# Kernel optimization log

Measured on AMD Instinct MI355X. Metric: run time of the kernel, lower is better.

Reference implementation:

```python
import jax, jax.numpy as jnp
import numpy as np

D = 1024
B, N = 4, 2048

def setup_inputs() -> dict:
    key = jax.random.key(0)
    ks = jax.random.split(key, 7)
    sc = 1.0 / np.sqrt(D)
    return {
        "x": jax.random.normal(ks[0], (B, N, D), dtype=jnp.float32),
        "wq_w": jax.random.normal(ks[1], (D, D), dtype=jnp.float32) * sc,
        "wq_b": jax.random.normal(ks[2], (D,), dtype=jnp.float32) * 0.01,
        "wk_w": jax.random.normal(ks[3], (D, D), dtype=jnp.float32) * sc,
        "wk_b": jax.random.normal(ks[4], (D,), dtype=jnp.float32) * 0.01,
        "wv_w": jax.random.normal(ks[5], (D, D), dtype=jnp.float32) * sc,
        "wv_b": jax.random.normal(ks[6], (D,), dtype=jnp.float32) * 0.01,
    }

def reference(x, wq_w, wq_b, wk_w, wk_b, wv_w, wv_b):
    # torch Linear: y = x @ W^T + b
    q = x @ wq_w.T + wq_b
    k = x @ wk_w.T + wk_b
    v = x @ wv_w.T + wv_b
    d = q.shape[-1]
    s = jnp.einsum("bid,bjd->bij", q, k) / jnp.sqrt(jnp.float32(d))
    # faithful to original: triu then transpose (zeros, NOT -inf, enter the softmax)
    t = jnp.swapaxes(jnp.triu(s), -2, -1)
    p = jax.nn.softmax(t, axis=-2)
    attn = jnp.swapaxes(jnp.triu(p), -2, -1) @ v
    return attn
```

## Files before the change

kernel.cpp:

```cpp
#include <hip/hip_runtime.h>
#include <hip/hip_fp16.h>
#include <cstdint>

typedef _Float16 half8_t __attribute__((ext_vector_type(8)));
typedef float f32x4 __attribute__((ext_vector_type(4)));

#define D_ 1024
#define B_ 4
#define N_ 2048
#define M_ (B_*N_)
#define NC_ 3072

#define OFF_WCAT  0u
#define OFF_BCAT  6291456u
#define OFF_XB    6303744u
#define OFF_Q     23080960u
#define OFF_K     39858176u
#define OFF_V     56635392u
#define OFF_ZP    73412608u
#define OFF_DEXP  74461184u
#define OFF_SV    74493952u
#define OFF_INVD  74756096u
#define OFF_CD    74788864u

__device__ __forceinline__ void gload_lds16(const void* g, void* l) {
  __builtin_amdgcn_global_load_lds(
      (const __attribute__((address_space(1))) unsigned int*)(uintptr_t)g,
      (__attribute__((address_space(3))) unsigned int*)(uintptr_t)l, 16, 0, 0);
}


__device__ __forceinline__ void calc_soff(int tid, int soff[4]) {
#pragma unroll
  for (int i = 0; i < 4; ++i) {
    int L = i * 8192 + tid * 16;
    int s = L >> 10;
    int w = L & 1023;
    w ^= ((w >> 9) & 1) << 5;
    int r  = (s >> 1) * 16 + (w >> 6);
    int kb = (s & 1) * 64 + (w & 63);
    soff[i] = r * 2048 + kb;
  }
}

#define MFMA_QUAD(QM, QN)                                                     \
  _Pragma("unroll")                                                           \
  for (int ks = 0; ks < 2; ++ks)                                              \
    _Pragma("unroll")                                                         \
    for (int mf = 0; mf < 4; ++mf)                                            \
      _Pragma("unroll")                                                       \
      for (int nf = 0; nf < 2; ++nf)                                          \
        acc[(QM)*4 + mf][(QN)*2 + nf] = __builtin_amdgcn_mfma_f32_16x16x32_f16( \
            a[mf][ks], b[(QN)][nf][ks], acc[(QM)*4 + mf][(QN)*2 + nf], 0, 0, 0);

__device__ __forceinline__ void gemm256_8ph(const char* Ag, const char* Bg,
                                            char* smem, f32x4 acc[8][4]) {
  const int tid  = threadIdx.x;
  const int lane = tid & 63;
  const int wave = tid >> 6;
  const int wm = wave >> 2, wn = wave & 3;

  int soff[4];
  calc_soff(tid, soff);
  const int wlane = (((lane & 15) * 64 + (lane >> 4) * 16)) ^ (((lane >> 3) & 1) << 5);

#pragma unroll
  for (int i = 0; i < 4; ++i) gload_lds16(Ag + soff[i], smem + i * 8192 + tid * 16);
#pragma unroll
  for (int i = 0; i < 4; ++i) gload_lds16(Bg + soff[i], smem + 32768 + i * 8192 + tid * 16);
  asm volatile("s_waitcnt vmcnt(0)" ::: "memory");
  __builtin_amdgcn_s_barrier();

  for (int t = 0; t < 16; ++t) {
    char* A0  = smem + ((t & 1) << 16);
    char* B0  = A0 + 32768;
    char* A1  = smem + (((t + 1) & 1) << 16);
    char* B1s = A1 + 32768;
    const half8_t* ap = (const half8_t*)(A0 + wm * 16384 + wlane);
    const half8_t* bp = (const half8_t*)(B0 + wn * 8192 + wlane);
    const char* Agn = Ag + (t + 1) * 128;
    const char* Bgn = Bg + (t + 1) * 128;
    const bool pre = (t < 15);

    half8_t a[4][2];
    half8_t b[2][2][2];

#pragma unroll
    for (int mf = 0; mf < 4; ++mf)
#pragma unroll
      for (int ks = 0; ks < 2; ++ks)
        a[mf][ks] = ap[(mf * 2 + ks) * 64];
#pragma unroll
    for (int nf = 0; nf < 2; ++nf)
#pragma unroll
      for (int ks = 0; ks < 2; ++ks)
        b[0][nf][ks] = bp[(nf * 2 + ks) * 64];
    if (pre) {
#pragma unroll
      for (int i = 0; i < 4; ++i) gload_lds16(Agn + soff[i], A1 + i * 8192 + tid * 16);
    }
    __builtin_amdgcn_s_barrier();
    asm volatile("s_waitcnt lgkmcnt(0)" ::: "memory");
    __builtin_amdgcn_s_setprio(1);
    MFMA_QUAD(0, 0)
    __builtin_amdgcn_s_setprio(0);
    __builtin_amdgcn_s_barrier();

#pragma unroll
    for (int nf = 0; nf < 2; ++nf)
#pragma unroll
      for (int ks = 0; ks < 2; ++ks)
        b[1][nf][ks] = bp[((2 + nf) * 2 + ks) * 64];
    if (pre) {
#pragma unroll
      for (int i = 0; i < 4; ++i) gload_lds16(Bgn + soff[i], B1s + i * 8192 + tid * 16);
    }
    __builtin_amdgcn_s_barrier();
    asm volatile("s_waitcnt lgkmcnt(0)" ::: "memory");
    __builtin_amdgcn_s_setprio(1);
    MFMA_QUAD(0, 1)
    __builtin_amdgcn_s_setprio(0);
    __builtin_amdgcn_s_barrier();

#pragma unroll
    for (int mf = 0; mf < 4; ++mf)
#pragma unroll
      for (int ks = 0; ks < 2; ++ks)
        a[mf][ks] = ap[((4 + mf) * 2 + ks) * 64];
    __builtin_amdgcn_s_barrier();
    asm volatile("s_waitcnt lgkmcnt(0)" ::: "memory");
    __builtin_amdgcn_s_setprio(1);
    MFMA_QUAD(1, 0)
    __builtin_amdgcn_s_setprio(0);
    __builtin_amdgcn_s_barrier();

    __builtin_amdgcn_s_setprio(1);
    MFMA_QUAD(1, 1)
    __builtin_amdgcn_s_setprio(0);
    if (pre) asm volatile("s_waitcnt vmcnt(0)" ::: "memory");
    __builtin_amdgcn_s_barrier();
  }
}

__global__ __launch_bounds__(256) void k_prep(
    const float* __restrict__ x, const float* __restrict__ wq, const float* __restrict__ wk,
    const float* __restrict__ wv, const float* __restrict__ bq, const float* __restrict__ bk,
    const float* __restrict__ bv, __half* __restrict__ xb, __half* __restrict__ wcat,
    float* __restrict__ bcat, float* __restrict__ Zpart) {
  const int NX4 = (M_ * D_) / 4;
  const int NW4 = (D_ * D_) / 4;
  const int TOT = NX4 + 3 * NW4;
  int tid0 = blockIdx.x * 256 + threadIdx.x;
  int stride = gridDim.x * 256;
  for (int i = tid0; i < TOT; i += stride) {
    float4 f; __half* dst;
    if (i < NX4) {
      f = ((const float4*)x)[i];
      dst = xb + 4 * (size_t)i;
    } else {
      int j = i - NX4; int w = j / NW4; int o = j - w * NW4;
      const float* src = (w == 0) ? wq : (w == 1) ? wk : wv;
      f = ((const float4*)src)[o];
      dst = wcat + (size_t)w * (D_ * D_) + 4 * (size_t)o;
    }
    __half h0 = __float2half(f.x), h1 = __float2half(f.y),
           h2 = __float2half(f.z), h3 = __float2half(f.w);
    ushort4 u = { __half_as_ushort(h0), __half_as_ushort(h1),
                  __half_as_ushort(h2), __half_as_ushort(h3) };
    *((ushort4*)dst) = u;
  }
  if (tid0 < NC_)
    bcat[tid0] = (tid0 < 1024) ? bq[tid0] : (tid0 < 2048) ? bk[tid0 - 1024] : bv[tid0 - 2048];
  for (int i = tid0; i < M_ * 32; i += stride) Zpart[i] = 0.f;
}

__global__ __launch_bounds__(512, 2) void k_qkv256(
    const __half* __restrict__ xb, const __half* __restrict__ wcat,
    const float* __restrict__ bcat,
    __half* __restrict__ q, __half* __restrict__ kx, __half* __restrict__ v) {
  __shared__ __align__(16) char smem[131072];
  int bid = blockIdx.x;
  int tile = (bid & 7) * 48 + (bid >> 3);
  int bm = tile / 12, bn = tile % 12;

  f32x4 acc[8][4];
#pragma unroll
  for (int i = 0; i < 8; ++i)
#pragma unroll
    for (int j = 0; j < 4; ++j) acc[i][j] = f32x4{0.f, 0.f, 0.f, 0.f};

  gemm256_8ph((const char*)(xb + (size_t)bm * 256 * D_),
              (const char*)(wcat + (size_t)bn * 256 * D_), smem, acc);

  const int lane = threadIdx.x & 63;
  const int wave = threadIdx.x >> 6;
  const int wm = wave >> 2, wn = wave & 3;
  int sel = bn >> 2;
  __half* outp = (sel == 0) ? q : (sel == 1) ? kx : v;
  int colbase = (bn & 3) * 256 + wn * 64;
#pragma unroll
  for (int nf = 0; nf < 4; ++nf) {
    int nloc = colbase + nf * 16 + (lane & 15);
    float bias = bcat[bn * 256 + wn * 64 + nf * 16 + (lane & 15)];
#pragma unroll
    for (int mf = 0; mf < 8; ++mf) {
#pragma unroll
      for (int rr = 0; rr < 4; ++rr) {
        int m = bm * 256 + wm * 128 + mf * 16 + (lane >> 4) * 4 + rr;
        outp[(size_t)m * D_ + nloc] = __float2half(acc[mf][nf][rr] + bias);
      }
    }
  }
}

__global__ __launch_bounds__(512, 2) void k_stats256(
    const __half* __restrict__ q, const __half* __restrict__ kx,
    float* __restrict__ Zpart, float* __restrict__ dexp) {
  __shared__ __align__(16) char smem[131072];
  int bid = blockIdx.x;
  int tile = (bid & 7) * 18 + (bid >> 3);
  int b = tile / 36;
  int r = tile % 36;
  int ti = 0;
  while (r >= 8 - ti) { r -= 8 - ti; ++ti; }
  int tj = ti + r;

  f32x4 acc[8][4];
#pragma unroll
  for (int i = 0; i < 8; ++i)
#pragma unroll
    for (int j = 0; j < 4; ++j) acc[i][j] = f32x4{0.f, 0.f, 0.f, 0.f};

  const size_t base = (size_t)b * N_ * D_;
  gemm256_8ph((const char*)(q + base + (size_t)ti * 256 * D_),
              (const char*)(kx + base + (size_t)tj * 256 * D_), smem, acc);

  const int lane = threadIdx.x & 63;
  const int wave = threadIdx.x >> 6;
  const int wm = wave >> 2, wn = wave & 3;
  const bool offd = (tj > ti);
  const float scale = 0.03125f;
  int zr0 = b * N_ + ti * 256;
#pragma unroll
  for (int mf = 0; mf < 8; ++mf) {
#pragma unroll
    for (int rr = 0; rr < 4; ++rr) {
      int il = wm * 128 + mf * 16 + (lane >> 4) * 4 + rr;
      float ssum = 0.f;
#pragma unroll
      for (int nf = 0; nf < 4; ++nf) {
        int jl = wn * 64 + nf * 16 + (lane & 15);
        float e = __expf(acc[mf][nf][rr] * scale);
        bool keep = offd || (jl >= il);
        if (!offd && jl == il) dexp[zr0 + il] = e;
        ssum += keep ? e : 0.f;
      }
      ssum += __shfl_xor(ssum, 1);
      ssum += __shfl_xor(ssum, 2);
      ssum += __shfl_xor(ssum, 4);
      ssum += __shfl_xor(ssum, 8);
      if ((lane & 15) == 0)
        Zpart[(size_t)(zr0 + il) * 32 + tj * 4 + wn] = ssum;
    }
  }
}

__global__ __launch_bounds__(256) void k_mid(
    const __half* __restrict__ v, const float* __restrict__ Zpart,
    const float* __restrict__ dexp, float* __restrict__ Sv,
    float* __restrict__ invD, float* __restrict__ cdiag) {
  int tid = blockIdx.x * 256 + threadIdx.x;
  int b = tid >> 14, c = (tid >> 10) & 15, d = tid & 1023;
  const __half* vp = v + ((size_t)(b * N_ + c * 128)) * D_ + d;
  float s = 0.f;
#pragma unroll 8
  for (int r2 = 0; r2 < 128; ++r2) s += __half2float(vp[(size_t)r2 * D_]);
  Sv[tid] = s;
  if (tid < M_) {
    float z = 0.f;
#pragma unroll
    for (int t = 0; t < 32; ++t) z += Zpart[(size_t)tid * 32 + t];
    float Dd = (float)(tid & (N_ - 1)) + z;
    float iv = 1.f / Dd;
    invD[tid] = iv;
    cdiag[tid] = dexp[tid] * iv;
  }
}

__global__ __launch_bounds__(256) void k_out(
    const __half* __restrict__ v, const float* __restrict__ Sv,
    const float* __restrict__ invD, const float* __restrict__ cdiag,
    float* __restrict__ out) {
  int tid = blockIdx.x * 256 + threadIdx.x;
  int b = tid >> 14, c = (tid >> 10) & 15, d = tid & 1023;
  float run = 0.f;
  for (int cc = 0; cc < c; ++cc) run += Sv[((b << 4) + cc) * 1024 + d];
  const __half* vp = v + ((size_t)(b * N_ + c * 128)) * D_ + d;
  float* op = out + ((size_t)(b * N_ + c * 128)) * D_ + d;
  int zi0 = b * N_ + c * 128;
#pragma unroll 4
  for (int r2 = 0; r2 < 128; ++r2) {
    float vi = __half2float(vp[(size_t)r2 * D_]);
    op[(size_t)r2 * D_] = run * invD[zi0 + r2] + cdiag[zi0 + r2] * vi;
    run += vi;
  }
}

extern "C" void kernel_launch(void* const* d_in, const int* in_sizes, int n_in,
                              void* d_out, int out_size, void* d_ws, size_t ws_size,
                              hipStream_t stream) {
  const float* x  = (const float*)d_in[0];
  const float* wq = (const float*)d_in[1];
  const float* bq = (const float*)d_in[2];
  const float* wk = (const float*)d_in[3];
  const float* bk = (const float*)d_in[4];
  const float* wv = (const float*)d_in[5];
  const float* bv = (const float*)d_in[6];
  float* out = (float*)d_out;
  char* ws = (char*)d_ws;

  __half* wcat = (__half*)(ws + OFF_WCAT);
  float*  bcat = (float*)(ws + OFF_BCAT);
  __half* xb   = (__half*)(ws + OFF_XB);
  __half* q    = (__half*)(ws + OFF_Q);
  __half* k    = (__half*)(ws + OFF_K);
  __half* v    = (__half*)(ws + OFF_V);
  float* Zpart = (float*)(ws + OFF_ZP);
  float* dexp  = (float*)(ws + OFF_DEXP);
  float* Sv    = (float*)(ws + OFF_SV);
  float* invD  = (float*)(ws + OFF_INVD);
  float* cdiag = (float*)(ws + OFF_CD);

  k_prep<<<dim3(2048), dim3(256), 0, stream>>>(x, wq, wk, wv, bq, bk, bv, xb, wcat, bcat, Zpart);
  k_qkv256<<<dim3(384), dim3(512), 0, stream>>>(xb, wcat, bcat, q, k, v);
  k_stats256<<<dim3(144), dim3(512), 0, stream>>>(q, k, Zpart, dexp);
  k_mid<<<dim3(256), dim3(256), 0, stream>>>(v, Zpart, dexp, Sv, invD, cdiag);
  k_out<<<dim3(256), dim3(256), 0, stream>>>(v, Sv, invD, cdiag, out);
}
```

Before: 142.3 us.

## Replace 256x256 QKV GEMM with simpler single-buffered 128x128 tile kernel

The QKV projection GEMM drops the 256x256, 512-thread, 8-phase pipelined tile kernel and uses a 128x128 tile with 256 threads and 32KB of LDS. Each 64-wide K slice is staged with an XOR swizzle and waited on before compute, with no double buffering. The grid grows from 384 to 1536 blocks and the block-to-tile swizzle is removed. This buys higher occupancy and simpler code, but loses the overlap of loads with MFMA work and reuses each loaded tile less.

```diff
diff --git a/kernel.cpp b/kernel.cpp
--- a/kernel.cpp
+++ b/kernel.cpp
@@ -29,6 +29,50 @@
       (__attribute__((address_space(3))) unsigned int*)(uintptr_t)l, 16, 0, 0);
 }
 
+__device__ __forceinline__ void stage128x64(const __half* rowbase, char* lds, int tid) {
+#pragma unroll
+  for (int inst = 0; inst < 4; ++inst) {
+    int L  = inst * 4096 + tid * 16;
+    int r  = L >> 7;
+    int cb = L & 127;
+    int cbs = cb ^ ((r & 7) << 4);
+    gload_lds16((const char*)rowbase + (size_t)r * (D_ * 2) + cbs, lds + L);
+  }
+}
+
+__device__ __forceinline__ half8_t ldsfrag(const char* lds, int row, int cbyte) {
+  int b = (row << 7) + (cbyte ^ ((row & 7) << 4));
+  return *reinterpret_cast<const half8_t*>(lds + b);
+}
+
+__device__ __forceinline__ void gemm128_core(const __half* Arow0, const __half* Brow0,
+                                             char* As, char* Bs, f32x4 acc[4][4]) {
+  const int tid  = threadIdx.x;
+  const int lane = tid & 63;
+  const int wave = tid >> 6;
+  const int wm = wave >> 1, wn = wave & 1;
+  for (int kt = 0; kt < 16; ++kt) {
+    if (kt) __syncthreads();
+    stage128x64(Arow0 + kt * 64, As, tid);
+    stage128x64(Brow0 + kt * 64, Bs, tid);
+    asm volatile("s_waitcnt vmcnt(0)" ::: "memory");
+    __syncthreads();
+#pragma unroll
+    for (int kk = 0; kk < 2; ++kk) {
+      const int cbyte = kk * 64 + (lane >> 4) * 16;
+      half8_t a[4], b[4];
+#pragma unroll
+      for (int mf = 0; mf < 4; ++mf) a[mf] = ldsfrag(As, wm * 64 + mf * 16 + (lane & 15), cbyte);
+#pragma unroll
+      for (int nf = 0; nf < 4; ++nf) b[nf] = ldsfrag(Bs, wn * 64 + nf * 16 + (lane & 15), cbyte);
+#pragma unroll
+      for (int mf = 0; mf < 4; ++mf)
+#pragma unroll
+        for (int nf = 0; nf < 4; ++nf)
+          acc[mf][nf] = __builtin_amdgcn_mfma_f32_16x16x32_f16(a[mf], b[nf], acc[mf][nf], 0, 0, 0);
+    }
+  }
+}
 
 __device__ __forceinline__ void calc_soff(int tid, int soff[4]) {
 #pragma unroll
@@ -174,40 +218,37 @@
   for (int i = tid0; i < M_ * 32; i += stride) Zpart[i] = 0.f;
 }
 
-__global__ __launch_bounds__(512, 2) void k_qkv256(
+__global__ __launch_bounds__(256) void k_qkv(
     const __half* __restrict__ xb, const __half* __restrict__ wcat,
     const float* __restrict__ bcat,
     __half* __restrict__ q, __half* __restrict__ kx, __half* __restrict__ v) {
-  __shared__ __align__(16) char smem[131072];
+  __shared__ __align__(16) char smem[32768];
+  char* As = smem; char* Bs = smem + 16384;
   int bid = blockIdx.x;
-  int tile = (bid & 7) * 48 + (bid >> 3);
-  int bm = tile / 12, bn = tile % 12;
-
-  f32x4 acc[8][4];
-#pragma unroll
-  for (int i = 0; i < 8; ++i)
+  int bm = bid / 24, bn = bid % 24;
+  f32x4 acc[4][4];
+#pragma unroll
+  for (int i = 0; i < 4; ++i)
 #pragma unroll
     for (int j = 0; j < 4; ++j) acc[i][j] = f32x4{0.f, 0.f, 0.f, 0.f};
-
-  gemm256_8ph((const char*)(xb + (size_t)bm * 256 * D_),
-              (const char*)(wcat + (size_t)bn * 256 * D_), smem, acc);
+  gemm128_core(xb + (size_t)bm * 128 * D_, wcat + (size_t)bn * 128 * D_, As, Bs, acc);
 
   const int lane = threadIdx.x & 63;
   const int wave = threadIdx.x >> 6;
-  const int wm = wave >> 2, wn = wave & 3;
-  int sel = bn >> 2;
+  const int wm = wave >> 1, wn = wave & 1;
+  int sel = bn >> 3;
   __half* outp = (sel == 0) ? q : (sel == 1) ? kx : v;
-  int colbase = (bn & 3) * 256 + wn * 64;
 #pragma unroll
   for (int nf = 0; nf < 4; ++nf) {
-    int nloc = colbase + nf * 16 + (lane & 15);
-    float bias = bcat[bn * 256 + wn * 64 + nf * 16 + (lane & 15)];
-#pragma unroll
-    for (int mf = 0; mf < 8; ++mf) {
-#pragma unroll
-      for (int rr = 0; rr < 4; ++rr) {
-        int m = bm * 256 + wm * 128 + mf * 16 + (lane >> 4) * 4 + rr;
-        outp[(size_t)m * D_ + nloc] = __float2half(acc[mf][nf][rr] + bias);
+    int nloc = wn * 64 + nf * 16 + (lane & 15);
+    float bias = bcat[bn * 128 + nloc];
+    int ncol = (bn & 7) * 128 + nloc;
+#pragma unroll
+    for (int mf = 0; mf < 4; ++mf) {
+#pragma unroll
+      for (int r = 0; r < 4; ++r) {
+        int m = bm * 128 + wm * 64 + mf * 16 + (lane >> 4) * 4 + r;
+        outp[(size_t)m * D_ + ncol] = __float2half(acc[mf][nf][r] + bias);
       }
     }
   }
@@ -332,7 +373,7 @@
   float* cdiag = (float*)(ws + OFF_CD);
 
   k_prep<<<dim3(2048), dim3(256), 0, stream>>>(x, wq, wk, wv, bq, bk, bv, xb, wcat, bcat, Zpart);
-  k_qkv256<<<dim3(384), dim3(512), 0, stream>>>(xb, wcat, bcat, q, k, v);
+  k_qkv<<<dim3(64 * 24), dim3(256), 0, stream>>>(xb, wcat, bcat, q, k, v);
   k_stats256<<<dim3(144), dim3(512), 0, stream>>>(q, k, Zpart, dexp);
   k_mid<<<dim3(256), dim3(256), 0, stream>>>(v, Zpart, dexp, Sv, invD, cdiag);
   k_out<<<dim3(256), dim3(256), 0, stream>>>(v, Sv, invD, cdiag, out);
```

Measured after the change: 137.4 us. 3.5% less time.
